# Kernel optimization log

Hardware: AMD Instinct MI355X
Metric: run time of the kernel (lower is better)

The kernel has to match this reference:

```python
import jax, jax.numpy as jnp
import numpy as np

E_MOD = 210000.0
NU = 0.3
_G = 1.0 / np.sqrt(3.0)
_XI = np.array([-_G, _G, _G, -_G])
_ETA = np.array([-_G, -_G, _G, _G])
# [gauss_point, local_node] shape-function derivative tables
DXI = (0.25 * np.stack([-(1 - _ETA), 1 - _ETA, 1 + _ETA, -(1 + _ETA)], axis=1)).astype(np.float32)
DETA = (0.25 * np.stack([-(1 - _XI), -(1 + _XI), 1 + _XI, 1 - _XI], axis=1)).astype(np.float32)

NE = 2048  # elements per side
NN = NE + 1  # nodes per side


def setup_inputs() -> dict:
    key = jax.random.key(0)
    xs = np.arange(NN, dtype=np.float32)
    gx, gy = np.meshgrid(xs, xs, indexing='ij')
    nodes = np.stack([gx.ravel(), gy.ravel()], axis=-1)  # [NN*NN, 2]
    r, c = np.meshgrid(np.arange(NE), np.arange(NE), indexing='ij')
    n00 = (r * NN + c + 1).astype(np.int32)  # 1-based node ids
    elements = np.stack([n00, n00 + 1, n00 + NN + 1, n00 + NN], axis=-1).reshape(-1, 4)
    disp = jax.random.normal(key, (2 * NN * NN,), dtype=jnp.float32) * 0.1
    bc_u_ids = (np.arange(NN, dtype=np.int64) * NN + 1).astype(np.int32)  # left edge
    bc_v_ids = (np.arange(NN, dtype=np.int64) + 1).astype(np.int32)  # bottom edge
    return {
        'disp': disp,
        'nodes': jnp.asarray(nodes),
        'elements': jnp.asarray(elements),
        'bc_u_ids': jnp.asarray(bc_u_ids),
        'bc_u_vals': jnp.zeros((NN,), jnp.float32),
        'bc_v_ids': jnp.asarray(bc_v_ids),
        'bc_v_vals': jnp.zeros((NN,), jnp.float32),
    }


def reference(disp, nodes, elements, bc_u_ids, bc_u_vals, bc_v_ids, bc_v_vals):
    dxi = jnp.asarray(DXI)   # [4 gp, 4 node]
    deta = jnp.asarray(DETA)
    idx = elements - 1  # [E,4] 0-based node indices
    u = disp[2 * idx]       # [E,4] x-displacements per local node
    v = disp[2 * idx + 1]   # [E,4] y-displacements per local node
    # bug-faithful source behavior: x2 uses local-node-0's u displacement
    xd_idx = idx[:, jnp.array([0, 0, 2, 3])]
    X = disp[2 * xd_idx] + nodes[idx, 0]  # [E,4] deformed x coords
    Y = v + nodes[idx, 1]                 # [E,4] deformed y coords
    # Jacobian entries per element per gauss point: [E,4gp]
    a = jnp.einsum('ij,ej->ei', dxi, X)
    b = jnp.einsum('ij,ej->ei', dxi, Y)
    c = jnp.einsum('ij,ej->ei', deta, X)
    d = jnp.einsum('ij,ej->ei', deta, Y)
    inv = 1.0 / (a * d - b * c)
    i11 = inv * d
    i12 = -inv * c
    i21 = -inv * b
    i22 = inv * a
    # Gauss-weight-summed B entries (weights are all 1): [E,4 node]
    B0e = jnp.einsum('ei,ij->ej', i11, dxi) + jnp.einsum('ei,ij->ej', i12, deta)  # B[0][2j] == B[2][2j]
    B1o = jnp.einsum('ei,ij->ej', i21, dxi) + jnp.einsum('ei,ij->ej', i22, deta)  # B[1][2j+1] == B[2][2j+1]
    # bug-faithful strains: the source loop overwrites, so only local node j=3 survives;
    # B[0][2j+1] and B[1][2j] are structurally zero.
    exx = B0e[:, 3] * u[:, 3]
    eyy = B1o[:, 3] * v[:, 3]
    gam = B0e[:, 3] * u[:, 3] + B1o[:, 3] * v[:, 3]
    k = E_MOD / (1.0 - NU * NU)
    sxx = k * (exx + NU * eyy)
    syy = k * (eyy + NU * exx)
    sxy = E_MOD / (1.0 + NU) * gam
    en = 0.5 * (exx * sxx + eyy * syy + 2.0 * gam * sxy)
    energy = jnp.sum(en * en)
    bc = (jnp.sum((disp[2 * (bc_u_ids - 1)] - bc_u_vals) ** 2)
          + jnp.sum((disp[2 * (bc_v_ids - 1) + 1] - bc_v_vals) ** 2))
    return energy + bc * 1e10
```

## Files before the change

### kernel.cpp

```cpp
#include <hip/hip_runtime.h>

#define NEc 2048
#define NNc 2049
#define VSTRIP 8
#define NROWG (NEc / VSTRIP)
#define NSTRIP (NROWG * NEc)
#define NTHR 256
#define NBLK (NSTRIP / NTHR)


__device__ __forceinline__ void quad_pt(float a, float b, float cc, float dd,
                                        float P, float N,
                                        float& B0a, float& B1a) {
    const float det = a * dd - b * cc;
    const float inv = __builtin_amdgcn_rcpf(det);
    B0a += inv * (dd * P + cc * N);
    B1a += inv * (a * N + b * P);
}

__global__ __launch_bounds__(NTHR) void fem_energy_kernel(
    const float* __restrict__ disp,
    const int* __restrict__ bc_u_ids, const float* __restrict__ bc_u_vals,
    const int* __restrict__ bc_v_ids, const float* __restrict__ bc_v_vals,
    double* __restrict__ partials)
{
    const float L = 0.10566243270259355f;
    const float H = 0.39433756729740645f;
    const float kmat = 210000.0f / (1.0f - 0.09f);
    const float gmat = 210000.0f / 1.3f;

    const int tid = blockIdx.x * NTHR + threadIdx.x;
    const int rg  = tid >> 11;
    const int c   = tid & (NEc - 1);
    int node = (rg * VSTRIP) * NNc + c;

    float local = 0.0f;

    float2 t0 = *reinterpret_cast<const float2*>(disp + 2 * node);
    float2 t1 = *reinterpret_cast<const float2*>(disp + 2 * node + 2);

#pragma unroll
    for (int k = 0; k < VSTRIP; ++k) {
        node += NNc;
        const float2 b0 = *reinterpret_cast<const float2*>(disp + 2 * node);
        const float2 b1 = *reinterpret_cast<const float2*>(disp + 2 * node + 2);
        const float d0u = t0.x, d0v = t0.y, d1v = t1.y;
        const float d3u = b0.x, d3v = b0.y, d2u = b1.x, d2v = b1.y;

        const float dA  = d2u - d3u;
        const float B1v = (d1v - d0v) + 1.0f;
        const float B2v = (d2v - d3v) + 1.0f;
        const float C1v = (d3u - d0u) + 1.0f;
        const float C2v = (d2u - d0u) + 1.0f;
        const float D1v = d3v - d0v;
        const float D2v = d2v - d1v;

        const float Bm = B2v - B1v, Cm = C1v - C2v, Dm = D1v - D2v;
        const float hB1 = 0.5f * B1v, hC2 = 0.5f * C2v, hD2 = 0.5f * D2v;
        const float bL = hB1 + L * Bm, bH = hB1 + H * Bm;
        const float cL = hC2 + L * Cm, cH = hC2 + H * Cm;
        const float dL = hD2 + L * Dm, dH = hD2 + H * Dm;
        const float aL = L * dA, aH = H * dA;

        float B0a = 0.0f, B1a = 0.0f;
        quad_pt(aL, bL, cH, dH, L, H, B0a, B1a);
        quad_pt(aL, bL, cL, dL, L, L, B0a, B1a);
        quad_pt(aH, bH, cL, dL, H, L, B0a, B1a);
        quad_pt(aH, bH, cH, dH, H, H, B0a, B1a);

        const float exx = -(B0a * d3u);
        const float eyy = B1a * d3v;
        const float gam = exx + eyy;
        const float sxx = kmat * (exx + 0.3f * eyy);
        const float syy = kmat * (eyy + 0.3f * exx);
        const float sxy = gmat * gam;
        const float en  = 0.5f * (exx * sxx + eyy * syy + 2.0f * gam * sxy);
        local += en * en;

        t0 = b0; t1 = b1;
    }

    if (tid < NNc) {
        const float du = disp[2 * (bc_u_ids[tid] - 1)]     - bc_u_vals[tid];
        const float dv = disp[2 * (bc_v_ids[tid] - 1) + 1] - bc_v_vals[tid];
        local += (du * du + dv * dv) * 1.0e10f;
    }

#pragma unroll
    for (int off = 32; off > 0; off >>= 1) local += __shfl_down(local, off, 64);
    __shared__ float wsum[NTHR / 64];
    const int lane = threadIdx.x & 63;
    const int wid  = threadIdx.x >> 6;
    if (lane == 0) wsum[wid] = local;
    __syncthreads();
    if (threadIdx.x == 0) {
        partials[blockIdx.x] = (double)(wsum[0] + wsum[1] + wsum[2] + wsum[3]);
    }
}

__global__ __launch_bounds__(256) void finalize_kernel(
    const double* __restrict__ partials, float* __restrict__ out)
{
    double s = 0.0;
    for (int i = threadIdx.x; i < NBLK; i += 256) s += partials[i];
#pragma unroll
    for (int off = 32; off > 0; off >>= 1) s += __shfl_down(s, off, 64);
    __shared__ double wsum[4];
    const int lane = threadIdx.x & 63;
    const int wid  = threadIdx.x >> 6;
    if (lane == 0) wsum[wid] = s;
    __syncthreads();
    if (threadIdx.x == 0) out[0] = (float)(wsum[0] + wsum[1] + wsum[2] + wsum[3]);
}

extern "C" void kernel_launch(void* const* d_in, const int* in_sizes, int n_in,
                              void* d_out, int out_size, void* d_ws, size_t ws_size,
                              hipStream_t stream) {
    const float* disp      = (const float*)d_in[0];
    const int*   bc_u_ids  = (const int*)d_in[3];
    const float* bc_u_vals = (const float*)d_in[4];
    const int*   bc_v_ids  = (const int*)d_in[5];
    const float* bc_v_vals = (const float*)d_in[6];
    double* partials = (double*)d_ws;

    fem_energy_kernel<<<NBLK, NTHR, 0, stream>>>(
        disp, bc_u_ids, bc_u_vals, bc_v_ids, bc_v_vals, partials);
    finalize_kernel<<<1, 256, 0, stream>>>(partials, (float*)d_out);
}
```

Baseline: 21.07 us.

## Process two adjacent columns per thread with wide preloaded row loads

Each thread now computes two horizontally adjacent elements per row, loading one float4 plus one float2 per node row and preloading all nine rows into registers before computing. This halves the thread count and shares the middle column's loads between both elements, reducing redundant global loads and per-thread overhead. The stress/energy formula is also simplified algebraically to a quadratic form with folded constants. It raises register pressure and halves available parallelism, which may lower occupancy.

```diff
diff --git a/kernel.cpp b/kernel.cpp
--- a/kernel.cpp
+++ b/kernel.cpp
@@ -3,11 +3,15 @@
 #define NEc 2048
 #define NNc 2049
 #define VSTRIP 8
+#define NCOLP 1024
 #define NROWG (NEc / VSTRIP)
-#define NSTRIP (NROWG * NEc)
 #define NTHR 256
-#define NBLK (NSTRIP / NTHR)
+#define NTOT (NROWG * NCOLP)
+#define NBLK (NTOT / NTHR)
 
+
+#define Lq 0.10566243270259355f
+#define Hq 0.39433756729740645f
 
 __device__ __forceinline__ void quad_pt(float a, float b, float cc, float dd,
                                         float P, float N,
@@ -18,66 +22,72 @@
     B1a += inv * (a * N + b * P);
 }
 
+__device__ __forceinline__ void element_energy(
+    float d0u, float d0v, float d1v,
+    float d3u, float d3v, float d2u, float d2v,
+    float CA, float CB, float& local)
+{
+    const float dA  = d2u - d3u;
+    const float B1v = (d1v - d0v) + 1.0f;
+    const float B2v = (d2v - d3v) + 1.0f;
+    const float C1v = (d3u - d0u) + 1.0f;
+    const float C2v = (d2u - d0u) + 1.0f;
+    const float D1v = d3v - d0v;
+    const float D2v = d2v - d1v;
+
+    const float Bm = B2v - B1v, Cm = C1v - C2v, Dm = D1v - D2v;
+    const float hB1 = 0.5f * B1v, hC2 = 0.5f * C2v, hD2 = 0.5f * D2v;
+    const float bL = hB1 + Lq * Bm, bH = hB1 + Hq * Bm;
+    const float cL = hC2 + Lq * Cm, cH = hC2 + Hq * Cm;
+    const float dL = hD2 + Lq * Dm, dH = hD2 + Hq * Dm;
+    const float aL = Lq * dA, aH = Hq * dA;
+
+    float B0a = 0.0f, B1a = 0.0f;
+    quad_pt(aL, bL, cH, dH, Lq, Hq, B0a, B1a);
+    quad_pt(aL, bL, cL, dL, Lq, Lq, B0a, B1a);
+    quad_pt(aH, bH, cL, dL, Hq, Lq, B0a, B1a);
+    quad_pt(aH, bH, cH, dH, Hq, Hq, B0a, B1a);
+
+    const float e   = B0a * d3u;
+    const float eyy = B1a * d3v;
+    const float en  = CA * (e * e + eyy * eyy) - CB * (e * eyy);
+    local += en * en;
+}
+
 __global__ __launch_bounds__(NTHR) void fem_energy_kernel(
     const float* __restrict__ disp,
     const int* __restrict__ bc_u_ids, const float* __restrict__ bc_u_vals,
     const int* __restrict__ bc_v_ids, const float* __restrict__ bc_v_vals,
     double* __restrict__ partials)
 {
-    const float L = 0.10566243270259355f;
-    const float H = 0.39433756729740645f;
     const float kmat = 210000.0f / (1.0f - 0.09f);
     const float gmat = 210000.0f / 1.3f;
+    const float CA = 0.5f * kmat + gmat;
+    const float CB = 0.3f * kmat + 2.0f * gmat;
 
     const int tid = blockIdx.x * NTHR + threadIdx.x;
-    const int rg  = tid >> 11;
-    const int c   = tid & (NEc - 1);
-    int node = (rg * VSTRIP) * NNc + c;
+    const int rg  = tid >> 10;
+    const int cp  = tid & (NCOLP - 1);
+    const int node0 = (rg * VSTRIP) * NNc + 2 * cp;
+
+    float4 rowA[VSTRIP + 1];
+    float2 rowB[VSTRIP + 1];
+#pragma unroll
+    for (int j = 0; j <= VSTRIP; ++j) {
+        const float* p = disp + 2 * (node0 + j * NNc);
+        rowA[j] = *reinterpret_cast<const float4*>(p);
+        rowB[j] = *reinterpret_cast<const float2*>(p + 4);
+    }
 
     float local = 0.0f;
-
-    float2 t0 = *reinterpret_cast<const float2*>(disp + 2 * node);
-    float2 t1 = *reinterpret_cast<const float2*>(disp + 2 * node + 2);
-
 #pragma unroll
     for (int k = 0; k < VSTRIP; ++k) {
-        node += NNc;
-        const float2 b0 = *reinterpret_cast<const float2*>(disp + 2 * node);
-        const float2 b1 = *reinterpret_cast<const float2*>(disp + 2 * node + 2);
-        const float d0u = t0.x, d0v = t0.y, d1v = t1.y;
-        const float d3u = b0.x, d3v = b0.y, d2u = b1.x, d2v = b1.y;
-
-        const float dA  = d2u - d3u;
-        const float B1v = (d1v - d0v) + 1.0f;
-        const float B2v = (d2v - d3v) + 1.0f;
-        const float C1v = (d3u - d0u) + 1.0f;
-        const float C2v = (d2u - d0u) + 1.0f;
-        const float D1v = d3v - d0v;
-        const float D2v = d2v - d1v;
-
-        const float Bm = B2v - B1v, Cm = C1v - C2v, Dm = D1v - D2v;
-        const float hB1 = 0.5f * B1v, hC2 = 0.5f * C2v, hD2 = 0.5f * D2v;
-        const float bL = hB1 + L * Bm, bH = hB1 + H * Bm;
-        const float cL = hC2 + L * Cm, cH = hC2 + H * Cm;
-        const float dL = hD2 + L * Dm, dH = hD2 + H * Dm;
-        const float aL = L * dA, aH = H * dA;
-
-        float B0a = 0.0f, B1a = 0.0f;
-        quad_pt(aL, bL, cH, dH, L, H, B0a, B1a);
-        quad_pt(aL, bL, cL, dL, L, L, B0a, B1a);
-        quad_pt(aH, bH, cL, dL, H, L, B0a, B1a);
-        quad_pt(aH, bH, cH, dH, H, H, B0a, B1a);
-
-        const float exx = -(B0a * d3u);
-        const float eyy = B1a * d3v;
-        const float gam = exx + eyy;
-        const float sxx = kmat * (exx + 0.3f * eyy);
-        const float syy = kmat * (eyy + 0.3f * exx);
-        const float sxy = gmat * gam;
-        const float en  = 0.5f * (exx * sxx + eyy * syy + 2.0f * gam * sxy);
-        local += en * en;
-
-        t0 = b0; t1 = b1;
+        const float4 top = rowA[k],     bot = rowA[k + 1];
+        const float2 tB  = rowB[k],     bB  = rowB[k + 1];
+        element_energy(top.x, top.y, top.w,
+                       bot.x, bot.y, bot.z, bot.w, CA, CB, local);
+        element_energy(top.z, top.w, tB.y,
+                       bot.z, bot.w, bB.x, bB.y, CA, CB, local);
     }
 
     if (tid < NNc) {
```

Result: slower. 21.53 us (+2.2%).
